# Kernel tuning notes

Hardware: AMD Instinct MI355X
Metric: run time of the kernel (lower is better)

The kernel has to match this reference:

```python
import jax, jax.numpy as jnp
import numpy as np

C1, C2, RATIO = 512, 256, 16

def setup_inputs() -> dict:
    key = jax.random.key(0)
    k1, k2, k3 = jax.random.split(key, 3)
    x = jax.random.normal(k1, (32, C1, 64, 64), dtype=jnp.float32)
    # torch Linear(c1, c1//ratio, bias=False): weight [c1//ratio, c1]
    w1 = jax.random.normal(k2, (C1 // RATIO, C1), dtype=jnp.float32) * (1.0 / np.sqrt(C1))
    w2 = jax.random.normal(k3, (C1, C1 // RATIO), dtype=jnp.float32) * (1.0 / np.sqrt(C1 // RATIO))
    return {"x": x, "w1": w1, "w2": w2}

def reference(x, w1, w2):
    b, c, h, w = x.shape
    # global average pool -> [b, c]
    y = jnp.mean(x, axis=(2, 3))
    # SE MLP: relu(y @ w1.T) @ w2.T, then sigmoid
    y = jax.nn.sigmoid(jnp.einsum('br,cr->bc', jax.nn.relu(jnp.einsum('bc,rc->br', y, w1)), w2))
    # descending sort indices over channels, keep top c2
    idx = jnp.argsort(-y, axis=1)[:, :C2]            # [b, c2] int
    # per-batch channel gather: out[b] = x[b, idx[b]]
    out = jnp.take_along_axis(x, idx[:, :, None, None], axis=1)  # [b, c2, h, w]
    return out
```

## Files before the change

### kernel.cpp

```cpp
#include <hip/hip_runtime.h>
#include <hip/hip_bf16.h>
#include <math.h>


#define C1 512
#define C2 256
#define CMID 32
#define HW 4096
#define B 32
#define W1PAD 516

typedef float f32x4 __attribute__((ext_vector_type(4)));

__device__ float g_y[B * C1];
__device__ int   g_rank[B * C1];

__global__ __launch_bounds__(256) void pool_np_kernel(const float* __restrict__ x) {
    if (blockIdx.x < 64) g_rank[blockIdx.x * 256 + threadIdx.x] = 0;

    int bc = blockIdx.x * 4 + (threadIdx.x >> 6);
    int L = threadIdx.x & 63;
    const float* a = x + (size_t)bc * HW;
    const float* base = a + (L >> 1) * 128 + (L & 1) * 4;
    f32x4 r = *(const f32x4*)base;
#pragma unroll
    for (int i = 1; i < 16; ++i) {
        f32x4 v = *(const f32x4*)(base + 8 * i);
        r.x = __fadd_rn(r.x, v.x);
        r.y = __fadd_rn(r.y, v.y);
        r.z = __fadd_rn(r.z, v.z);
        r.w = __fadd_rn(r.w, v.w);
    }
    float s = __fadd_rn(__fadd_rn(r.x, r.y), __fadd_rn(r.z, r.w));
    s = __fadd_rn(s, __shfl_xor(s, 1));
    s = __fadd_rn(s, __shfl_xor(s, 2));
    s = __fadd_rn(s, __shfl_xor(s, 4));
    s = __fadd_rn(s, __shfl_xor(s, 8));
    s = __fadd_rn(s, __shfl_xor(s, 16));
    s = __fadd_rn(s, __shfl_xor(s, 32));
    if (L == 0) g_y[bc] = __fdiv_rn(s, 4096.0f);
}

__global__ __launch_bounds__(512) void se_rank_kernel(const float* __restrict__ w1,
                                                      const float* __restrict__ w2) {
    int b = blockIdx.x >> 3;
    int j = blockIdx.x & 7;
    int t = threadIdx.x;
    __shared__ float ys[C1];
    __shared__ float hs[CMID];
    __shared__ float ss[C1];
    __shared__ float w1s[CMID * W1PAD];

    f32x4 w2r[8];
#pragma unroll
    for (int i = 0; i < 8; ++i)
        w2r[i] = ((const f32x4*)(w2 + t * CMID))[i];

#pragma unroll
    for (int i = 0; i < 8; ++i) {
        int u = i * 512 + t;
        int row  = u >> 7;
        int col4 = u & 127;
        f32x4 v = ((const f32x4*)w1)[u];
        *(f32x4*)&w1s[row * W1PAD + col4 * 4] = v;
    }
    ys[t] = g_y[b * C1 + t];
    __syncthreads();

    if (t < CMID * 4) {
        int row = t >> 2, k = t & 3;
        const float* wr = &w1s[row * W1PAD];
        float Lk = 0.f;
#pragma unroll
        for (int c = 0; c < C1; c += 8) {
            Lk = __fadd_rn(Lk, __fmul_rn(ys[c + k],     wr[c + k]));
            Lk = __fadd_rn(Lk, __fmul_rn(ys[c + 4 + k], wr[c + 4 + k]));
        }
        Lk = __fadd_rn(Lk, __shfl_xor(Lk, 1));
        Lk = __fadd_rn(Lk, __shfl_xor(Lk, 2));
        if (k == 0) hs[row] = Lk > 0.0f ? Lk : 0.0f;
    }
    __syncthreads();

    {
        float L0 = 0.f, L1 = 0.f, L2 = 0.f, L3 = 0.f;
#pragma unroll
        for (int i = 0; i < 8; i += 2) {
            L0 = __fadd_rn(L0, __fmul_rn(hs[i * 4 + 0], w2r[i].x));
            L1 = __fadd_rn(L1, __fmul_rn(hs[i * 4 + 1], w2r[i].y));
            L2 = __fadd_rn(L2, __fmul_rn(hs[i * 4 + 2], w2r[i].z));
            L3 = __fadd_rn(L3, __fmul_rn(hs[i * 4 + 3], w2r[i].w));
            L0 = __fadd_rn(L0, __fmul_rn(hs[i * 4 + 4], w2r[i + 1].x));
            L1 = __fadd_rn(L1, __fmul_rn(hs[i * 4 + 5], w2r[i + 1].y));
            L2 = __fadd_rn(L2, __fmul_rn(hs[i * 4 + 6], w2r[i + 1].z));
            L3 = __fadd_rn(L3, __fmul_rn(hs[i * 4 + 7], w2r[i + 1].w));
        }
        float z = __fadd_rn(__fadd_rn(L0, L1), __fadd_rn(L2, L3));
        float e = (float)exp((double)(-z));
        ss[t] = __fdiv_rn(1.0f, __fadd_rn(1.0f, e));
    }
    __syncthreads();

    {
        float sc = ss[t];
        int c0 = j * 64;
        int rank = 0;
#pragma unroll 16
        for (int c = c0; c < c0 + 64; ++c) {
            float v = ss[c];
            rank += (int)((v > sc) || (v == sc && c < t));
        }
        atomicAdd(&g_rank[b * C1 + t], rank);
    }
}

__global__ __launch_bounds__(512) void gather_kernel(const float* __restrict__ x,
                                                     float* __restrict__ out) {
    int bid = blockIdx.x;
    int b = bid >> 8;
    int r = bid & 255;
    int t = threadIdx.x;
    __shared__ int win;
    int rk = g_rank[b * C1 + t];
    if (rk == r) win = t;
    __syncthreads();
    int c = win;
    const f32x4* src = (const f32x4*)(x + ((size_t)(b * C1 + c)) * HW);
    f32x4* dst = (f32x4*)(out + (size_t)bid * HW);
    f32x4 v0 = src[t];
    f32x4 v1 = src[t + 512];
    __builtin_nontemporal_store(v0, &dst[t]);
    __builtin_nontemporal_store(v1, &dst[t + 512]);
}

extern "C" void kernel_launch(void* const* d_in, const int* in_sizes, int n_in,
                              void* d_out, int out_size, void* d_ws, size_t ws_size,
                              hipStream_t stream) {
    const float* x  = (const float*)d_in[0];
    const float* w1 = (const float*)d_in[1];
    const float* w2 = (const float*)d_in[2];
    float* out = (float*)d_out;

    pool_np_kernel<<<B * C1 / 4, 256, 0, stream>>>(x);
    se_rank_kernel<<<B * 8, 512, 0, stream>>>(w1, w2);
    gather_kernel<<<B * C2, 512, 0, stream>>>(x, out);
}
```

Before: 90.46 us.

## Fuse pooling and SE ranking into one kernel with atomic completion counter

Merges the pooling and SE/rank kernels into one launch. The first 2048 blocks pool eight channels each and bump a global done-counter; the trailing 256 blocks spin on that counter, then run the MLP and rank. The SE path drops the shared-memory staging of w1 and reads w1 directly from global memory. This removes one kernel launch boundary and the large w1 shared-memory allocation, at the risk of spinning blocks occupying CUs, and depends on the pool blocks being scheduled before the SE blocks to avoid deadlock. The counter is reset inside the gather kernel.

```diff
diff --git a/kernel.cpp b/kernel.cpp
--- a/kernel.cpp
+++ b/kernel.cpp
@@ -8,109 +8,120 @@
 #define CMID 32
 #define HW 4096
 #define B 32
-#define W1PAD 516
+#define GRID_POOL 2048
+#define GRID_SE   256
 
 typedef float f32x4 __attribute__((ext_vector_type(4)));
 
 __device__ float g_y[B * C1];
 __device__ int   g_rank[B * C1];
+__device__ unsigned g_pool_done = 0;
 
-__global__ __launch_bounds__(256) void pool_np_kernel(const float* __restrict__ x) {
-    if (blockIdx.x < 64) g_rank[blockIdx.x * 256 + threadIdx.x] = 0;
-
-    int bc = blockIdx.x * 4 + (threadIdx.x >> 6);
-    int L = threadIdx.x & 63;
-    const float* a = x + (size_t)bc * HW;
-    const float* base = a + (L >> 1) * 128 + (L & 1) * 4;
-    f32x4 r = *(const f32x4*)base;
-#pragma unroll
-    for (int i = 1; i < 16; ++i) {
-        f32x4 v = *(const f32x4*)(base + 8 * i);
-        r.x = __fadd_rn(r.x, v.x);
-        r.y = __fadd_rn(r.y, v.y);
-        r.z = __fadd_rn(r.z, v.z);
-        r.w = __fadd_rn(r.w, v.w);
-    }
-    float s = __fadd_rn(__fadd_rn(r.x, r.y), __fadd_rn(r.z, r.w));
-    s = __fadd_rn(s, __shfl_xor(s, 1));
-    s = __fadd_rn(s, __shfl_xor(s, 2));
-    s = __fadd_rn(s, __shfl_xor(s, 4));
-    s = __fadd_rn(s, __shfl_xor(s, 8));
-    s = __fadd_rn(s, __shfl_xor(s, 16));
-    s = __fadd_rn(s, __shfl_xor(s, 32));
-    if (L == 0) g_y[bc] = __fdiv_rn(s, 4096.0f);
-}
-
-__global__ __launch_bounds__(512) void se_rank_kernel(const float* __restrict__ w1,
-                                                      const float* __restrict__ w2) {
-    int b = blockIdx.x >> 3;
-    int j = blockIdx.x & 7;
-    int t = threadIdx.x;
+__global__ __launch_bounds__(512, 8) void pool_se_kernel(const float* __restrict__ x,
+                                                         const float* __restrict__ w1,
+                                                         const float* __restrict__ w2) {
     __shared__ float ys[C1];
     __shared__ float hs[CMID];
     __shared__ float ss[C1];
-    __shared__ float w1s[CMID * W1PAD];
+    int t = threadIdx.x;
 
-    f32x4 w2r[8];
+    if (blockIdx.x < GRID_POOL) {
+        if (blockIdx.x < 32) g_rank[blockIdx.x * 512 + t] = 0;
+
+        int wv = t >> 6;
+        int L  = t & 63;
+        int bc = blockIdx.x * 8 + wv;
+        const float* a = x + (size_t)bc * HW;
+        const float* base = a + (L >> 1) * 128 + (L & 1) * 4;
+        f32x4 r = *(const f32x4*)base;
 #pragma unroll
-    for (int i = 0; i < 8; ++i)
-        w2r[i] = ((const f32x4*)(w2 + t * CMID))[i];
+        for (int i = 1; i < 16; ++i) {
+            f32x4 v = *(const f32x4*)(base + 8 * i);
+            r.x = __fadd_rn(r.x, v.x);
+            r.y = __fadd_rn(r.y, v.y);
+            r.z = __fadd_rn(r.z, v.z);
+            r.w = __fadd_rn(r.w, v.w);
+        }
+        float s = __fadd_rn(__fadd_rn(r.x, r.y), __fadd_rn(r.z, r.w));
+        s = __fadd_rn(s, __shfl_xor(s, 1));
+        s = __fadd_rn(s, __shfl_xor(s, 2));
+        s = __fadd_rn(s, __shfl_xor(s, 4));
+        s = __fadd_rn(s, __shfl_xor(s, 8));
+        s = __fadd_rn(s, __shfl_xor(s, 16));
+        s = __fadd_rn(s, __shfl_xor(s, 32));
+        if (L == 0) g_y[bc] = __fdiv_rn(s, 4096.0f);
 
+        __syncthreads();
+        if (t == 0) {
+            __threadfence();
+            __hip_atomic_fetch_add(&g_pool_done, 1, __ATOMIC_ACQ_REL,
+                                   __HIP_MEMORY_SCOPE_AGENT);
+        }
+    } else {
+        int sb = blockIdx.x - GRID_POOL;
+        int b = sb >> 3;
+        int j = sb & 7;
+
+        f32x4 w2r[8];
 #pragma unroll
-    for (int i = 0; i < 8; ++i) {
-        int u = i * 512 + t;
-        int row  = u >> 7;
-        int col4 = u & 127;
-        f32x4 v = ((const f32x4*)w1)[u];
-        *(f32x4*)&w1s[row * W1PAD + col4 * 4] = v;
-    }
-    ys[t] = g_y[b * C1 + t];
-    __syncthreads();
+        for (int i = 0; i < 8; ++i)
+            w2r[i] = ((const f32x4*)(w2 + t * CMID))[i];
 
-    if (t < CMID * 4) {
-        int row = t >> 2, k = t & 3;
-        const float* wr = &w1s[row * W1PAD];
-        float Lk = 0.f;
+        if (t == 0) {
+            while (__hip_atomic_load(&g_pool_done, __ATOMIC_ACQUIRE,
+                                     __HIP_MEMORY_SCOPE_AGENT) < GRID_POOL)
+                __builtin_amdgcn_s_sleep(2);
+        }
+        __syncthreads();
+
+        ys[t] = g_y[b * C1 + t];
+        __syncthreads();
+
+        if (t < CMID * 4) {
+            int row = t >> 2, k = t & 3;
+            const float* v = w1 + row * C1;
+            float Lk = 0.f;
 #pragma unroll
-        for (int c = 0; c < C1; c += 8) {
-            Lk = __fadd_rn(Lk, __fmul_rn(ys[c + k],     wr[c + k]));
-            Lk = __fadd_rn(Lk, __fmul_rn(ys[c + 4 + k], wr[c + 4 + k]));
+            for (int c = 0; c < C1; c += 8) {
+                Lk = __fadd_rn(Lk, __fmul_rn(ys[c + k],     v[c + k]));
+                Lk = __fadd_rn(Lk, __fmul_rn(ys[c + 4 + k], v[c + 4 + k]));
+            }
+            Lk = __fadd_rn(Lk, __shfl_xor(Lk, 1));
+            Lk = __fadd_rn(Lk, __shfl_xor(Lk, 2));
+            if (k == 0) hs[row] = Lk > 0.0f ? Lk : 0.0f;
         }
-        Lk = __fadd_rn(Lk, __shfl_xor(Lk, 1));
-        Lk = __fadd_rn(Lk, __shfl_xor(Lk, 2));
-        if (k == 0) hs[row] = Lk > 0.0f ? Lk : 0.0f;
-    }
-    __syncthreads();
+        __syncthreads();
 
-    {
-        float L0 = 0.f, L1 = 0.f, L2 = 0.f, L3 = 0.f;
+        {
+            float L0 = 0.f, L1 = 0.f, L2 = 0.f, L3 = 0.f;
 #pragma unroll
-        for (int i = 0; i < 8; i += 2) {
-            L0 = __fadd_rn(L0, __fmul_rn(hs[i * 4 + 0], w2r[i].x));
-            L1 = __fadd_rn(L1, __fmul_rn(hs[i * 4 + 1], w2r[i].y));
-            L2 = __fadd_rn(L2, __fmul_rn(hs[i * 4 + 2], w2r[i].z));
-            L3 = __fadd_rn(L3, __fmul_rn(hs[i * 4 + 3], w2r[i].w));
-            L0 = __fadd_rn(L0, __fmul_rn(hs[i * 4 + 4], w2r[i + 1].x));
-            L1 = __fadd_rn(L1, __fmul_rn(hs[i * 4 + 5], w2r[i + 1].y));
-            L2 = __fadd_rn(L2, __fmul_rn(hs[i * 4 + 6], w2r[i + 1].z));
-            L3 = __fadd_rn(L3, __fmul_rn(hs[i * 4 + 7], w2r[i + 1].w));
+            for (int i = 0; i < 8; i += 2) {
+                L0 = __fadd_rn(L0, __fmul_rn(hs[i * 4 + 0], w2r[i].x));
+                L1 = __fadd_rn(L1, __fmul_rn(hs[i * 4 + 1], w2r[i].y));
+                L2 = __fadd_rn(L2, __fmul_rn(hs[i * 4 + 2], w2r[i].z));
+                L3 = __fadd_rn(L3, __fmul_rn(hs[i * 4 + 3], w2r[i].w));
+                L0 = __fadd_rn(L0, __fmul_rn(hs[i * 4 + 4], w2r[i + 1].x));
+                L1 = __fadd_rn(L1, __fmul_rn(hs[i * 4 + 5], w2r[i + 1].y));
+                L2 = __fadd_rn(L2, __fmul_rn(hs[i * 4 + 6], w2r[i + 1].z));
+                L3 = __fadd_rn(L3, __fmul_rn(hs[i * 4 + 7], w2r[i + 1].w));
+            }
+            float z = __fadd_rn(__fadd_rn(L0, L1), __fadd_rn(L2, L3));
+            float e = (float)exp((double)(-z));
+            ss[t] = __fdiv_rn(1.0f, __fadd_rn(1.0f, e));
         }
-        float z = __fadd_rn(__fadd_rn(L0, L1), __fadd_rn(L2, L3));
-        float e = (float)exp((double)(-z));
-        ss[t] = __fdiv_rn(1.0f, __fadd_rn(1.0f, e));
-    }
-    __syncthreads();
+        __syncthreads();
 
-    {
-        float sc = ss[t];
-        int c0 = j * 64;
-        int rank = 0;
+        {
+            float sc = ss[t];
+            int c0 = j * 64;
+            int rank = 0;
 #pragma unroll 16
-        for (int c = c0; c < c0 + 64; ++c) {
-            float v = ss[c];
-            rank += (int)((v > sc) || (v == sc && c < t));
+            for (int c = c0; c < c0 + 64; ++c) {
+                float v = ss[c];
+                rank += (int)((v > sc) || (v == sc && c < t));
+            }
+            atomicAdd(&g_rank[b * C1 + t], rank);
         }
-        atomicAdd(&g_rank[b * C1 + t], rank);
     }
 }
 
@@ -120,6 +131,8 @@
     int b = bid >> 8;
     int r = bid & 255;
     int t = threadIdx.x;
+    if (bid == 0 && t == 0)
+        __hip_atomic_store(&g_pool_done, 0, __ATOMIC_RELAXED, __HIP_MEMORY_SCOPE_AGENT);
     __shared__ int win;
     int rk = g_rank[b * C1 + t];
     if (rk == r) win = t;
@@ -141,7 +154,6 @@
     const float* w2 = (const float*)d_in[2];
     float* out = (float*)d_out;
 
-    pool_np_kernel<<<B * C1 / 4, 256, 0, stream>>>(x);
-    se_rank_kernel<<<B * 8, 512, 0, stream>>>(w1, w2);
+    pool_se_kernel<<<GRID_POOL + GRID_SE, 512, 0, stream>>>(x, w1, w2);
     gather_kernel<<<B * C2, 512, 0, stream>>>(x, out);
 }
```

Measured after the change: 263.0 us. 191% more time.
